# Kernel optimization log

Hardware: AMD Instinct MI355X
Metric: run time of the kernel (lower is better)

The kernel has to match this reference:

```python
import jax, jax.numpy as jnp
import numpy as np

# OmniNet(deepqmc) reconstruction: ElectronicSchNet v1 (2 interactions, kernel_dim=8,
# embedding_dim=16, dist_feat_dim=4) + Linear(16,1,bias=False) orbital + sum over electrons.
# SchNet v1: shared w and g per interaction, spin-dependent h (same/anti), nuclear
# messages via learned nuclear embeddings Y. Subnets: w = 2-layer log-DNN 4->6->8 with SSP,
# h = Linear(16,8), g = Linear(8,16). SSP(x) = softplus(x) - log(2).

N_UP, N_DOWN = 16, 16
N_ELEC = N_UP + N_DOWN
N_ATOMS = 8
DIST_FEAT, KERNEL, EMBED = 4, 8, 16
N_INTER = 2
BATCH = 4096


def ssp(x):
    return jax.nn.softplus(x) - jnp.log(2.0).astype(x.dtype)


def setup_inputs() -> dict:
    key = jax.random.key(0)
    ks = jax.random.split(key, 16)
    s = 0.5  # init scale
    return {
        'dists_nuc': jax.random.uniform(ks[0], (BATCH, N_ELEC, N_ATOMS, DIST_FEAT), jnp.float32),
        'dists_elec': jax.random.uniform(ks[1], (BATCH, N_ELEC, N_ELEC, DIST_FEAT), jnp.float32),
        'X': jax.random.normal(ks[2], (1, EMBED), jnp.float32) * s,          # electron embedding (n_up==n_down)
        'Y': jax.random.normal(ks[3], (N_ATOMS, KERNEL), jnp.float32) * s,   # nuclear embeddings
        'w1': jax.random.normal(ks[4], (N_INTER, DIST_FEAT, 6), jnp.float32) * s,
        'wb1': jax.random.normal(ks[5], (N_INTER, 6), jnp.float32) * s,
        'w2': jax.random.normal(ks[6], (N_INTER, 6, KERNEL), jnp.float32) * s,
        'wb2': jax.random.normal(ks[7], (N_INTER, KERNEL), jnp.float32) * s,
        'hs_w': jax.random.normal(ks[8], (N_INTER, EMBED, KERNEL), jnp.float32) * s,
        'hs_b': jax.random.normal(ks[9], (N_INTER, KERNEL), jnp.float32) * s,
        'ha_w': jax.random.normal(ks[10], (N_INTER, EMBED, KERNEL), jnp.float32) * s,
        'ha_b': jax.random.normal(ks[11], (N_INTER, KERNEL), jnp.float32) * s,
        'g_w': jax.random.normal(ks[12], (N_INTER, KERNEL, EMBED), jnp.float32) * s,
        'g_b': jax.random.normal(ks[13], (N_INTER, EMBED), jnp.float32) * s,
        'orb_w': jax.random.normal(ks[14], (EMBED,), jnp.float32) * s,
    }


def reference(dists_nuc, dists_elec, X, Y, w1, wb1, w2, wb2, hs_w, hs_b, ha_w, ha_b, g_w, g_b, orb_w):
    B, n_elec = dists_elec.shape[:2]
    dt = dists_elec.dtype
    spins = jnp.concatenate([jnp.zeros(N_UP, jnp.int32), jnp.ones(N_DOWN, jnp.int32)])
    eye = jnp.eye(n_elec, dtype=bool)
    same = ((spins[:, None] == spins[None, :]) & ~eye).astype(dt)  # (i,j) same-spin, no self
    anti = (spins[:, None] != spins[None, :]).astype(dt)

    # initial embeddings: all electrons share X[0] since n_up == n_down
    x = jnp.broadcast_to(X[0], (B, n_elec, EMBED))

    for n in range(N_INTER):
        def w_net(e):  # (..., 4) -> (..., 8)
            return ssp(e @ w1[n] + wb1[n]) @ w2[n] + wb2[n]
        we = w_net(dists_elec)            # (B, i, j, K)
        wn = w_net(dists_nuc)             # (B, i, M, K)
        hs = x @ hs_w[n] + hs_b[n]        # (B, j, K) same-spin message features
        ha = x @ ha_w[n] + ha_b[n]        # (B, j, K) anti-spin
        z = (jnp.einsum('bijk,ij,bjk->bik', we, same, hs)
             + jnp.einsum('bijk,ij,bjk->bik', we, anti, ha)
             + jnp.einsum('bimk,mk->bik', wn, Y))
        x = x + (z @ g_w[n] + g_b[n])     # residual update

    # orbital projection (Linear(16,1,bias=False)), squeeze, sum over electrons
    return (x @ orb_w).sum(axis=-1)       # (B,)
```

## Files before the change

### kernel.cpp

```cpp
#include <hip/hip_runtime.h>

#define NE 32
#define NA 8
#define DF 4
#define KD 8
#define ED 16
#define BATCH 4096

__device__ __forceinline__ float exp2_fast(float v) { return __builtin_amdgcn_exp2f(v); }
__device__ __forceinline__ float log2_fast(float v) { return __builtin_amdgcn_logf(v); }

__device__ __forceinline__ void wnet1(const float4 e,
                                      const float* __restrict__ B1s,
                                      const float* __restrict__ pW1,
                                      const float* __restrict__ pW2,
                                      const float* __restrict__ B2h,
                                      float* __restrict__ racc)
{
    const float LOG2E = 1.4426950408889634f;
    const float ex = e.x * LOG2E, ey = e.y * LOG2E;
    const float ez = e.z * LOG2E, ew = e.w * LOG2E;
    float r[6];
    #pragma unroll
    for (int a = 0; a < 6; ++a) {
        float u = B1s[a];
        u = fmaf(ex, pW1[0 * 6 + a], u);
        u = fmaf(ey, pW1[1 * 6 + a], u);
        u = fmaf(ez, pW1[2 * 6 + a], u);
        u = fmaf(ew, pW1[3 * 6 + a], u);
        r[a] = log2_fast(exp2_fast(u) + 1.0f);
    }
    #pragma unroll
    for (int k = 0; k < KD; ++k) {
        float acc = B2h[k];
        #pragma unroll
        for (int a = 0; a < 6; ++a) acc = fmaf(r[a], pW2[a * KD + k], acc);
        racc[k] = acc;
    }
}

__global__ __launch_bounds__(128, 4) void omni_kernel(
    const float* __restrict__ dists_nuc,
    const float* __restrict__ dists_elec,
    const float* __restrict__ X,
    const float* __restrict__ Y,
    const float* __restrict__ w1,
    const float* __restrict__ wb1,
    const float* __restrict__ w2,
    const float* __restrict__ wb2,
    const float* __restrict__ hs_w,
    const float* __restrict__ hs_b,
    const float* __restrict__ ha_w,
    const float* __restrict__ ha_b,
    const float* __restrict__ g_w,
    const float* __restrict__ g_b,
    const float* __restrict__ orb_w,
    float* __restrict__ out)
{
    const int tid  = threadIdx.x;
    const int h    = tid >> 6;
    const int lane = tid & 63;
    const int il   = lane & 15;
    const int jh   = lane >> 4;
    const int ig   = 16 * h + il;
    const int b    = blockIdx.x;
    const int sj   = jh >> 1;
    const int t32  = (sj == h) ? 0 : 32;

    __shared__ float msg[2][65][KD];
    __shared__ float part[2];

    if (tid < 16) msg[tid >> 3][64][tid & 7] = 0.0f;

    float x[ED];
    #pragma unroll
    for (int c = 0; c < ED; ++c) x[c] = X[c];

    const float* de = dists_elec + (((size_t)b * NE + ig) * NE + 8 * jh) * DF;
    const float* dn = dists_nuc  + (((size_t)b * NE + ig) * NA + 2 * jh) * DF;

    const float LOG2E = 1.4426950408889634f;
    const float LN2   = 0.6931471805599453f;

    #pragma unroll 1
    for (int n = 0; n < 2; ++n) {
        const float* pW1 = w1  + n * DF * 6;
        const float* pB1 = wb1 + n * 6;
        const float* pW2 = w2  + n * 6 * KD;
        const float* pB2 = wb2 + n * KD;

        float B1s[6];
        #pragma unroll
        for (int a = 0; a < 6; ++a) B1s[a] = pB1[a] * LOG2E;

        float B2h[KD];
        #pragma unroll
        for (int k = 0; k < KD; ++k) {
            float sw = pW2[k];
            #pragma unroll
            for (int a = 1; a < 6; ++a) sw += pW2[a * KD + k];
            B2h[k] = fmaf(pB2[k], LOG2E, -sw);
        }

        {
            float ms[KD], ma[KD];
            #pragma unroll
            for (int k = 0; k < KD; ++k) { ms[k] = hs_b[n * KD + k]; ma[k] = ha_b[n * KD + k]; }
            #pragma unroll
            for (int c = 0; c < ED; ++c) {
                const float xc = x[c];
                #pragma unroll
                for (int k = 0; k < KD; ++k) {
                    ms[k] = fmaf(xc, hs_w[n * ED * KD + c * KD + k], ms[k]);
                    ma[k] = fmaf(xc, ha_w[n * ED * KD + c * KD + k], ma[k]);
                }
            }
            if (jh == 0) {
                #pragma unroll
                for (int k = 0; k < KD; ++k) msg[n][ig][k] = ms[k];
            } else if (jh == 2) {
                #pragma unroll
                for (int k = 0; k < KD; ++k) msg[n][32 + ig][k] = ma[k];
            }
            __syncthreads();
        }

        float z[KD];
        #pragma unroll
        for (int k = 0; k < KD; ++k) z[k] = 0.0f;

        #pragma unroll
        for (int s = 0; s < 8; ++s) {
            const int j = 8 * jh + s;
            const float4 e = ((const float4*)de)[s];
            float racc[KD];
            wnet1(e, B1s, pW1, pW2, B2h, racc);
            const int row = (j == ig) ? 64 : (t32 + j);
            const float4 m0 = *(const float4*)&msg[n][row][0];
            const float4 m1 = *(const float4*)&msg[n][row][4];
            z[0] = fmaf(racc[0], m0.x, z[0]);
            z[1] = fmaf(racc[1], m0.y, z[1]);
            z[2] = fmaf(racc[2], m0.z, z[2]);
            z[3] = fmaf(racc[3], m0.w, z[3]);
            z[4] = fmaf(racc[4], m1.x, z[4]);
            z[5] = fmaf(racc[5], m1.y, z[5]);
            z[6] = fmaf(racc[6], m1.z, z[6]);
            z[7] = fmaf(racc[7], m1.w, z[7]);
        }

        #pragma unroll
        for (int t = 0; t < 2; ++t) {
            const int m = 2 * jh + t;
            const float4 e = ((const float4*)dn)[t];
            float racc[KD];
            wnet1(e, B1s, pW1, pW2, B2h, racc);
            const float4 y0 = ((const float4*)Y)[m * 2];
            const float4 y1 = ((const float4*)Y)[m * 2 + 1];
            z[0] = fmaf(racc[0], y0.x, z[0]);
            z[1] = fmaf(racc[1], y0.y, z[1]);
            z[2] = fmaf(racc[2], y0.z, z[2]);
            z[3] = fmaf(racc[3], y0.w, z[3]);
            z[4] = fmaf(racc[4], y1.x, z[4]);
            z[5] = fmaf(racc[5], y1.y, z[5]);
            z[6] = fmaf(racc[6], y1.z, z[6]);
            z[7] = fmaf(racc[7], y1.w, z[7]);
        }

        #pragma unroll
        for (int k = 0; k < KD; ++k) {
            z[k] += __shfl_xor(z[k], 16, 64);
            z[k] += __shfl_xor(z[k], 32, 64);
            z[k] *= LN2;
        }

        #pragma unroll
        for (int c = 0; c < ED; ++c) {
            float acc = g_b[n * ED + c];
            #pragma unroll
            for (int k = 0; k < KD; ++k)
                acc = fmaf(z[k], g_w[n * KD * ED + k * ED + c], acc);
            x[c] += acc;
        }
    }

    float dot = 0.0f;
    #pragma unroll
    for (int c = 0; c < ED; ++c) dot = fmaf(x[c], orb_w[c], dot);
    dot *= 0.25f;
    #pragma unroll
    for (int off = 1; off < 64; off <<= 1) dot += __shfl_xor(dot, off, 64);
    if (lane == 0) part[h] = dot;
    __syncthreads();
    if (tid == 0) out[b] = part[0] + part[1];
}

extern "C" void kernel_launch(void* const* d_in, const int* in_sizes, int n_in,
                              void* d_out, int out_size, void* d_ws, size_t ws_size,
                              hipStream_t stream) {
    const float* dists_nuc  = (const float*)d_in[0];
    const float* dists_elec = (const float*)d_in[1];
    const float* X     = (const float*)d_in[2];
    const float* Y     = (const float*)d_in[3];
    const float* w1    = (const float*)d_in[4];
    const float* wb1   = (const float*)d_in[5];
    const float* w2    = (const float*)d_in[6];
    const float* wb2   = (const float*)d_in[7];
    const float* hs_w  = (const float*)d_in[8];
    const float* hs_b  = (const float*)d_in[9];
    const float* ha_w  = (const float*)d_in[10];
    const float* ha_b  = (const float*)d_in[11];
    const float* g_w   = (const float*)d_in[12];
    const float* g_b   = (const float*)d_in[13];
    const float* orb_w = (const float*)d_in[14];
    float* out = (float*)d_out;

    dim3 grid(BATCH), block(128);
    omni_kernel<<<grid, block, 0, stream>>>(dists_nuc, dists_elec, X, Y,
                                            w1, wb1, w2, wb2,
                                            hs_w, hs_b, ha_w, ha_b,
                                            g_w, g_b, orb_w, out);
}
```

Measured before the change: 167.7 us.

## Fold weight-only products into a setup kernel and simplify interaction algebra

A small setup kernel now precomputes the weight-only products: the pre-scaled w-net weights and biases, the layer-1 message vectors from the constant embedding, and composed matrices g_w·h_w and g_w·orb_w. The main kernel then runs the first interaction without shared-memory messages, because all electrons share one embedding and the message reduces to a masked sum times a constant vector. It also computes the second-layer messages directly from the reduced z, and replaces the final embedding dot product with precomposed projections. Distance inputs are loaded once and reused across both interactions. The cost is an extra kernel launch and more live registers for the cached distance vectors.

New measurement: 156.3 us. -6.8%, faster.

```diff
diff --git a/kernel.cpp b/kernel.cpp
--- a/kernel.cpp
+++ b/kernel.cpp
@@ -7,54 +7,108 @@
 #define ED 16
 #define BATCH 4096
 
-__device__ __forceinline__ float exp2_fast(float v) { return __builtin_amdgcn_exp2f(v); }
-__device__ __forceinline__ float log2_fast(float v) { return __builtin_amdgcn_logf(v); }
-
-__device__ __forceinline__ void wnet1(const float4 e,
-                                      const float* __restrict__ B1s,
-                                      const float* __restrict__ pW1,
-                                      const float* __restrict__ pW2,
-                                      const float* __restrict__ B2h,
-                                      float* __restrict__ racc)
+#define WS_W1S0 0
+#define WS_W1S1 24
+#define WS_B1S0 48
+#define WS_B1S1 54
+#define WS_B2H0 60
+#define WS_B2H1 68
+#define WS_MS0  76
+#define WS_MA0  84
+#define WS_MS   92
+#define WS_MA   156
+#define WS_CS   220
+#define WS_CA   228
+#define WS_GO0  236
+#define WS_GO1  244
+#define WS_BASE 252
+
+__global__ void omni_setup(const float* __restrict__ X,   const float* __restrict__ w1,
+                           const float* __restrict__ wb1, const float* __restrict__ w2,
+                           const float* __restrict__ wb2, const float* __restrict__ hs_w,
+                           const float* __restrict__ hs_b,const float* __restrict__ ha_w,
+                           const float* __restrict__ ha_b,const float* __restrict__ g_w,
+                           const float* __restrict__ g_b, const float* __restrict__ orb_w,
+                           float* __restrict__ ws)
 {
-    const float LOG2E = 1.4426950408889634f;
-    const float ex = e.x * LOG2E, ey = e.y * LOG2E;
-    const float ez = e.z * LOG2E, ew = e.w * LOG2E;
+    const int t = threadIdx.x;
+    const float L   = 1.4426950408889634f;
+    const float LN2 = 0.6931471805599453f;
+    if (t < 48) {
+        ws[t] = w1[t] * L;
+    } else if (t < 60) {
+        ws[t] = wb1[t - 48] * L;
+    } else if (t < 76) {
+        const int u = t - 60, n = u >> 3, k = u & 7;
+        float sw = 0.f;
+        for (int a = 0; a < 6; ++a) sw += w2[n * 48 + a * KD + k];
+        ws[t] = wb2[n * KD + k] * L - sw;
+    } else if (t < 92) {
+        const int u = t - 76, tab = u >> 3, k = u & 7;
+        const float* mw = tab ? ha_w : hs_w;
+        const float* mb = tab ? ha_b : hs_b;
+        float acc = mb[k];
+        for (int c = 0; c < ED; ++c) acc += X[c] * mw[c * KD + k];
+        ws[t] = acc;
+    } else if (t < 220) {
+        int u = t - 92; const int tab = u >> 6; u &= 63;
+        const int kp = u >> 3, k = u & 7;
+        const float* mw = (tab ? ha_w : hs_w) + ED * KD;
+        float acc = 0.f;
+        for (int c = 0; c < ED; ++c)
+            acc += LN2 * g_w[kp * ED + c] * mw[c * KD + k];
+        ws[t] = acc;
+    } else if (t < 236) {
+        const int u = t - 220, tab = u >> 3, k = u & 7;
+        const float* mw = (tab ? ha_w : hs_w) + ED * KD;
+        const float* mb = (tab ? ha_b : hs_b) + KD;
+        float acc = mb[k];
+        for (int c = 0; c < ED; ++c) acc += (X[c] + g_b[c]) * mw[c * KD + k];
+        ws[t] = acc;
+    } else if (t < 252) {
+        const int u = t - 236, n = u >> 3, k = u & 7;
+        float acc = 0.f;
+        for (int c = 0; c < ED; ++c)
+            acc += LN2 * g_w[n * KD * ED + k * ED + c] * orb_w[c];
+        ws[t] = acc;
+    } else if (t == 252) {
+        float acc = 0.f;
+        for (int c = 0; c < ED; ++c) acc += (X[c] + g_b[c] + g_b[ED + c]) * orb_w[c];
+        ws[t] = acc;
+    }
+}
+
+__device__ __forceinline__ void wnet(const float4 e,
+                                     const float* __restrict__ vB1s,
+                                     const float* __restrict__ vB2h,
+                                     const float* __restrict__ sW1,
+                                     const float* __restrict__ sW2,
+                                     float* __restrict__ racc)
+{
     float r[6];
     #pragma unroll
     for (int a = 0; a < 6; ++a) {
-        float u = B1s[a];
-        u = fmaf(ex, pW1[0 * 6 + a], u);
-        u = fmaf(ey, pW1[1 * 6 + a], u);
-        u = fmaf(ez, pW1[2 * 6 + a], u);
-        u = fmaf(ew, pW1[3 * 6 + a], u);
-        r[a] = log2_fast(exp2_fast(u) + 1.0f);
+        float u = fmaf(e.x, sW1[a], vB1s[a]);
+        u = fmaf(e.y, sW1[6 + a], u);
+        u = fmaf(e.z, sW1[12 + a], u);
+        u = fmaf(e.w, sW1[18 + a], u);
+        r[a] = __builtin_amdgcn_logf(__builtin_amdgcn_exp2f(u) + 1.0f);
     }
     #pragma unroll
     for (int k = 0; k < KD; ++k) {
-        float acc = B2h[k];
-        #pragma unroll
-        for (int a = 0; a < 6; ++a) acc = fmaf(r[a], pW2[a * KD + k], acc);
+        float acc = fmaf(r[0], sW2[k], vB2h[k]);
+        #pragma unroll
+        for (int a = 1; a < 6; ++a) acc = fmaf(r[a], sW2[a * KD + k], acc);
         racc[k] = acc;
     }
 }
 
-__global__ __launch_bounds__(128, 4) void omni_kernel(
+__global__ __launch_bounds__(128, 4) void omni_main(
     const float* __restrict__ dists_nuc,
     const float* __restrict__ dists_elec,
-    const float* __restrict__ X,
     const float* __restrict__ Y,
-    const float* __restrict__ w1,
-    const float* __restrict__ wb1,
     const float* __restrict__ w2,
-    const float* __restrict__ wb2,
-    const float* __restrict__ hs_w,
-    const float* __restrict__ hs_b,
-    const float* __restrict__ ha_w,
-    const float* __restrict__ ha_b,
-    const float* __restrict__ g_w,
-    const float* __restrict__ g_b,
-    const float* __restrict__ orb_w,
+    const float* __restrict__ ws,
     float* __restrict__ out)
 {
     const int tid  = threadIdx.x;
@@ -65,127 +119,146 @@
     const int ig   = 16 * h + il;
     const int b    = blockIdx.x;
     const int sj   = jh >> 1;
-    const int t32  = (sj == h) ? 0 : 32;
-
-    __shared__ float msg[2][65][KD];
+    const bool same = (sj == h);
+    const int t32  = same ? 0 : 32;
+
+    __shared__ float msg[65][KD];
     __shared__ float part[2];
-
-    if (tid < 16) msg[tid >> 3][64][tid & 7] = 0.0f;
-
-    float x[ED];
-    #pragma unroll
-    for (int c = 0; c < ED; ++c) x[c] = X[c];
+    if (tid < KD) msg[64][tid] = 0.0f;
 
     const float* de = dists_elec + (((size_t)b * NE + ig) * NE + 8 * jh) * DF;
     const float* dn = dists_nuc  + (((size_t)b * NE + ig) * NA + 2 * jh) * DF;
-
-    const float LOG2E = 1.4426950408889634f;
-    const float LN2   = 0.6931471805599453f;
-
-    #pragma unroll 1
-    for (int n = 0; n < 2; ++n) {
-        const float* pW1 = w1  + n * DF * 6;
-        const float* pB1 = wb1 + n * 6;
-        const float* pW2 = w2  + n * 6 * KD;
-        const float* pB2 = wb2 + n * KD;
-
-        float B1s[6];
-        #pragma unroll
-        for (int a = 0; a < 6; ++a) B1s[a] = pB1[a] * LOG2E;
-
-        float B2h[KD];
-        #pragma unroll
-        for (int k = 0; k < KD; ++k) {
-            float sw = pW2[k];
-            #pragma unroll
-            for (int a = 1; a < 6; ++a) sw += pW2[a * KD + k];
-            B2h[k] = fmaf(pB2[k], LOG2E, -sw);
-        }
-
+    float4 E[8];
+    #pragma unroll
+    for (int s = 0; s < 8; ++s) E[s] = ((const float4*)de)[s];
+    const float4 F0 = ((const float4*)dn)[0];
+    const float4 F1 = ((const float4*)dn)[1];
+    const float4 Ya0 = ((const float4*)Y)[4 * jh + 0];
+    const float4 Ya1 = ((const float4*)Y)[4 * jh + 1];
+    const float4 Yb0 = ((const float4*)Y)[4 * jh + 2];
+    const float4 Yb1 = ((const float4*)Y)[4 * jh + 3];
+
+    float zr0[KD];
+    {
+        float vB1s[6], vB2h[KD], msel[KD];
+        #pragma unroll
+        for (int a = 0; a < 6; ++a) vB1s[a] = ws[WS_B1S0 + a];
+        #pragma unroll
+        for (int k = 0; k < KD; ++k) vB2h[k] = ws[WS_B2H0 + k];
+        #pragma unroll
+        for (int k = 0; k < KD; ++k) msel[k] = same ? ws[WS_MS0 + k] : ws[WS_MA0 + k];
+
+        float zacc[KD];
+        #pragma unroll
+        for (int k = 0; k < KD; ++k) zacc[k] = 0.0f;
+        const int scnt = ig - 8 * jh;
+        #pragma unroll
+        for (int s = 0; s < 8; ++s) {
+            float racc[KD];
+            wnet(E[s], vB1s, vB2h, ws + WS_W1S0, w2, racc);
+            const float mf = (s == scnt) ? 0.0f : 1.0f;
+            #pragma unroll
+            for (int k = 0; k < KD; ++k) zacc[k] = fmaf(racc[k], mf, zacc[k]);
+        }
+        float z[KD];
+        #pragma unroll
+        for (int k = 0; k < KD; ++k) z[k] = zacc[k] * msel[k];
         {
-            float ms[KD], ma[KD];
-            #pragma unroll
-            for (int k = 0; k < KD; ++k) { ms[k] = hs_b[n * KD + k]; ma[k] = ha_b[n * KD + k]; }
-            #pragma unroll
-            for (int c = 0; c < ED; ++c) {
-                const float xc = x[c];
-                #pragma unroll
-                for (int k = 0; k < KD; ++k) {
-                    ms[k] = fmaf(xc, hs_w[n * ED * KD + c * KD + k], ms[k]);
-                    ma[k] = fmaf(xc, ha_w[n * ED * KD + c * KD + k], ma[k]);
-                }
-            }
-            if (jh == 0) {
-                #pragma unroll
-                for (int k = 0; k < KD; ++k) msg[n][ig][k] = ms[k];
-            } else if (jh == 2) {
-                #pragma unroll
-                for (int k = 0; k < KD; ++k) msg[n][32 + ig][k] = ma[k];
-            }
-            __syncthreads();
-        }
-
-        float z[KD];
-        #pragma unroll
-        for (int k = 0; k < KD; ++k) z[k] = 0.0f;
-
-        #pragma unroll
-        for (int s = 0; s < 8; ++s) {
-            const int j = 8 * jh + s;
-            const float4 e = ((const float4*)de)[s];
-            float racc[KD];
-            wnet1(e, B1s, pW1, pW2, B2h, racc);
-            const int row = (j == ig) ? 64 : (t32 + j);
-            const float4 m0 = *(const float4*)&msg[n][row][0];
-            const float4 m1 = *(const float4*)&msg[n][row][4];
-            z[0] = fmaf(racc[0], m0.x, z[0]);
-            z[1] = fmaf(racc[1], m0.y, z[1]);
-            z[2] = fmaf(racc[2], m0.z, z[2]);
-            z[3] = fmaf(racc[3], m0.w, z[3]);
-            z[4] = fmaf(racc[4], m1.x, z[4]);
-            z[5] = fmaf(racc[5], m1.y, z[5]);
-            z[6] = fmaf(racc[6], m1.z, z[6]);
-            z[7] = fmaf(racc[7], m1.w, z[7]);
-        }
-
-        #pragma unroll
-        for (int t = 0; t < 2; ++t) {
-            const int m = 2 * jh + t;
-            const float4 e = ((const float4*)dn)[t];
-            float racc[KD];
-            wnet1(e, B1s, pW1, pW2, B2h, racc);
-            const float4 y0 = ((const float4*)Y)[m * 2];
-            const float4 y1 = ((const float4*)Y)[m * 2 + 1];
-            z[0] = fmaf(racc[0], y0.x, z[0]);
-            z[1] = fmaf(racc[1], y0.y, z[1]);
-            z[2] = fmaf(racc[2], y0.z, z[2]);
-            z[3] = fmaf(racc[3], y0.w, z[3]);
-            z[4] = fmaf(racc[4], y1.x, z[4]);
-            z[5] = fmaf(racc[5], y1.y, z[5]);
-            z[6] = fmaf(racc[6], y1.z, z[6]);
-            z[7] = fmaf(racc[7], y1.w, z[7]);
-        }
-
+            float racc[KD];
+            wnet(F0, vB1s, vB2h, ws + WS_W1S0, w2, racc);
+            z[0] = fmaf(racc[0], Ya0.x, z[0]); z[1] = fmaf(racc[1], Ya0.y, z[1]);
+            z[2] = fmaf(racc[2], Ya0.z, z[2]); z[3] = fmaf(racc[3], Ya0.w, z[3]);
+            z[4] = fmaf(racc[4], Ya1.x, z[4]); z[5] = fmaf(racc[5], Ya1.y, z[5]);
+            z[6] = fmaf(racc[6], Ya1.z, z[6]); z[7] = fmaf(racc[7], Ya1.w, z[7]);
+            wnet(F1, vB1s, vB2h, ws + WS_W1S0, w2, racc);
+            z[0] = fmaf(racc[0], Yb0.x, z[0]); z[1] = fmaf(racc[1], Yb0.y, z[1]);
+            z[2] = fmaf(racc[2], Yb0.z, z[2]); z[3] = fmaf(racc[3], Yb0.w, z[3]);
+            z[4] = fmaf(racc[4], Yb1.x, z[4]); z[5] = fmaf(racc[5], Yb1.y, z[5]);
+            z[6] = fmaf(racc[6], Yb1.z, z[6]); z[7] = fmaf(racc[7], Yb1.w, z[7]);
+        }
         #pragma unroll
         for (int k = 0; k < KD; ++k) {
             z[k] += __shfl_xor(z[k], 16, 64);
             z[k] += __shfl_xor(z[k], 32, 64);
-            z[k] *= LN2;
-        }
-
-        #pragma unroll
-        for (int c = 0; c < ED; ++c) {
-            float acc = g_b[n * ED + c];
-            #pragma unroll
-            for (int k = 0; k < KD; ++k)
-                acc = fmaf(z[k], g_w[n * KD * ED + k * ED + c], acc);
-            x[c] += acc;
+            zr0[k] = z[k];
+        }
+    }
+
+    {
+        float ms[KD], ma[KD];
+        #pragma unroll
+        for (int k = 0; k < KD; ++k) {
+            float as = zr0[0] * ws[WS_MS + k];
+            float aa = zr0[0] * ws[WS_MA + k];
+            #pragma unroll
+            for (int kp = 1; kp < KD; ++kp) {
+                as = fmaf(zr0[kp], ws[WS_MS + kp * KD + k], as);
+                aa = fmaf(zr0[kp], ws[WS_MA + kp * KD + k], aa);
+            }
+            ms[k] = as + ws[WS_CS + k];
+            ma[k] = aa + ws[WS_CA + k];
+        }
+        if (jh == 0) {
+            #pragma unroll
+            for (int k = 0; k < KD; ++k) msg[ig][k] = ms[k];
+        } else if (jh == 2) {
+            #pragma unroll
+            for (int k = 0; k < KD; ++k) msg[32 + ig][k] = ma[k];
+        }
+        __syncthreads();
+    }
+
+    float zr1[KD];
+    {
+        float vB1s[6], vB2h[KD];
+        #pragma unroll
+        for (int a = 0; a < 6; ++a) vB1s[a] = ws[WS_B1S1 + a];
+        #pragma unroll
+        for (int k = 0; k < KD; ++k) vB2h[k] = ws[WS_B2H1 + k];
+
+        float z[KD];
+        #pragma unroll
+        for (int k = 0; k < KD; ++k) z[k] = 0.0f;
+        #pragma unroll
+        for (int s = 0; s < 8; ++s) {
+            float racc[KD];
+            wnet(E[s], vB1s, vB2h, ws + WS_W1S1, w2 + 48, racc);
+            const int j = 8 * jh + s;
+            const int row = (j == ig) ? 64 : (t32 + j);
+            const float4 m0 = *(const float4*)&msg[row][0];
+            const float4 m1 = *(const float4*)&msg[row][4];
+            z[0] = fmaf(racc[0], m0.x, z[0]); z[1] = fmaf(racc[1], m0.y, z[1]);
+            z[2] = fmaf(racc[2], m0.z, z[2]); z[3] = fmaf(racc[3], m0.w, z[3]);
+            z[4] = fmaf(racc[4], m1.x, z[4]); z[5] = fmaf(racc[5], m1.y, z[5]);
+            z[6] = fmaf(racc[6], m1.z, z[6]); z[7] = fmaf(racc[7], m1.w, z[7]);
+        }
+        {
+            float racc[KD];
+            wnet(F0, vB1s, vB2h, ws + WS_W1S1, w2 + 48, racc);
+            z[0] = fmaf(racc[0], Ya0.x, z[0]); z[1] = fmaf(racc[1], Ya0.y, z[1]);
+            z[2] = fmaf(racc[2], Ya0.z, z[2]); z[3] = fmaf(racc[3], Ya0.w, z[3]);
+            z[4] = fmaf(racc[4], Ya1.x, z[4]); z[5] = fmaf(racc[5], Ya1.y, z[5]);
+            z[6] = fmaf(racc[6], Ya1.z, z[6]); z[7] = fmaf(racc[7], Ya1.w, z[7]);
+            wnet(F1, vB1s, vB2h, ws + WS_W1S1, w2 + 48, racc);
+            z[0] = fmaf(racc[0], Yb0.x, z[0]); z[1] = fmaf(racc[1], Yb0.y, z[1]);
+            z[2] = fmaf(racc[2], Yb0.z, z[2]); z[3] = fmaf(racc[3], Yb0.w, z[3]);
+            z[4] = fmaf(racc[4], Yb1.x, z[4]); z[5] = fmaf(racc[5], Yb1.y, z[5]);
+            z[6] = fmaf(racc[6], Yb1.z, z[6]); z[7] = fmaf(racc[7], Yb1.w, z[7]);
+        }
+        #pragma unroll
+        for (int k = 0; k < KD; ++k) {
+            z[k] += __shfl_xor(z[k], 16, 64);
+            z[k] += __shfl_xor(z[k], 32, 64);
+            zr1[k] = z[k];
         }
     }
 
     float dot = 0.0f;
     #pragma unroll
-    for (int c = 0; c < ED; ++c) dot = fmaf(x[c], orb_w[c], dot);
+    for (int k = 0; k < KD; ++k) dot = fmaf(zr0[k], ws[WS_GO0 + k], dot);
+    #pragma unroll
+    for (int k = 0; k < KD; ++k) dot = fmaf(zr1[k], ws[WS_GO1 + k], dot);
+    dot += ws[WS_BASE];
     dot *= 0.25f;
     #pragma unroll
     for (int off = 1; off < 64; off <<= 1) dot += __shfl_xor(dot, off, 64);
@@ -213,10 +286,9 @@
     const float* g_b   = (const float*)d_in[13];
     const float* orb_w = (const float*)d_in[14];
     float* out = (float*)d_out;
-
-    dim3 grid(BATCH), block(128);
-    omni_kernel<<<grid, block, 0, stream>>>(dists_nuc, dists_elec, X, Y,
-                                            w1, wb1, w2, wb2,
-                                            hs_w, hs_b, ha_w, ha_b,
-                                            g_w, g_b, orb_w, out);
-}
+    float* ws  = (float*)d_ws;
+
+    omni_setup<<<1, 256, 0, stream>>>(X, w1, wb1, w2, wb2, hs_w, hs_b,
+                                      ha_w, ha_b, g_w, g_b, orb_w, ws);
+    omni_main<<<BATCH, 128, 0, stream>>>(dists_nuc, dists_elec, Y, w2, ws, out);
+}
```
